# Performance work log

Measured on AMD Instinct MI355X. Metric: run time of the kernel, lower is better.

Reference implementation:

```python
import jax, jax.numpy as jnp
import numpy as np

RATIOS = (0.5, 1.0, 2.0)
SCALES = (8.0, 16.0, 32.0)
BASE = 7.0
FEAT = 16
N_PRE = 6000    # pre-NMS top-k (test-mode default of standard ProposalCreator)
N_POST = 300    # post-NMS proposals per image (fixed -> jit-safe padded output)
NMS_T = 0.7
MIN_SIZE = 16.0
SCALE = 1.0     # forward arg `scale` default
NA = 9          # len(ratios)*len(anchor_scales)


def anchor_base():
    ab = np.zeros((NA, 4), np.float32)
    for i, r in enumerate(RATIOS):
        for j, s in enumerate(SCALES):
            h = BASE * s * np.sqrt(r)
            w = BASE * s * np.sqrt(1.0 / r)
            k = i * len(SCALES) + j
            ab[k] = [BASE / 2 - h / 2, BASE / 2 - w / 2, BASE / 2 + h / 2, BASE / 2 + w / 2]
    return jnp.asarray(ab)


def enum_anchors(H, W):
    # positions-major ordering: (H*W, 9, 4) -> (H*W*9, 4), matching permute(0,2,3,1)
    ab = anchor_base()
    sy = jnp.arange(H, dtype=jnp.float32) * FEAT
    sx = jnp.arange(W, dtype=jnp.float32) * FEAT
    ys, xs = jnp.meshgrid(sy, sx, indexing='ij')
    shift = jnp.stack([ys.ravel(), xs.ravel(), ys.ravel(), xs.ravel()], axis=1)
    return (shift[:, None, :] + ab[None, :, :]).reshape(-1, 4)


def conv2d(x, w, b, pad):
    y = jax.lax.conv_general_dilated(x, w, (1, 1), pad,
                                     dimension_numbers=('NCHW', 'OIHW', 'NCHW'))
    return y + b[None, :, None, None]


def decode(anchors, loc):
    ah = anchors[:, 2] - anchors[:, 0]
    aw = anchors[:, 3] - anchors[:, 1]
    acy = anchors[:, 0] + 0.5 * ah
    acx = anchors[:, 1] + 0.5 * aw
    dy, dx, dh, dw = loc[:, 0], loc[:, 1], loc[:, 2], loc[:, 3]
    cy = dy * ah + acy
    cx = dx * aw + acx
    h = jnp.exp(dh) * ah
    w = jnp.exp(dw) * aw
    return jnp.stack([cy - 0.5 * h, cx - 0.5 * w, cy + 0.5 * h, cx + 0.5 * w], axis=1)


def iou_matrix(b):
    tl = jnp.maximum(b[:, None, :2], b[None, :, :2])
    br = jnp.minimum(b[:, None, 2:], b[None, :, 2:])
    inter = jnp.prod(jnp.clip(br - tl, 0.0, None), axis=-1)
    area = jnp.prod(b[:, 2:] - b[:, :2], axis=-1)
    return inter / (area[:, None] + area[None, :] - inter + 1e-9)


def propose(loc, fg, anchors, img_h, img_w):
    boxes = decode(anchors, loc)
    boxes = jnp.stack([jnp.clip(boxes[:, 0], 0.0, img_h),
                       jnp.clip(boxes[:, 1], 0.0, img_w),
                       jnp.clip(boxes[:, 2], 0.0, img_h),
                       jnp.clip(boxes[:, 3], 0.0, img_w)], axis=1)
    hs = boxes[:, 2] - boxes[:, 0]
    ws = boxes[:, 3] - boxes[:, 1]
    ms = MIN_SIZE * SCALE
    valid = (hs >= ms) & (ws >= ms)
    score = jnp.where(valid, fg, -jnp.inf)
    _, idx = jax.lax.top_k(score, N_PRE)          # sorted by score desc
    bk = boxes[idx]                                # [N_PRE, 4]
    iou = iou_matrix(bk)                           # [N_PRE, N_PRE]

    def body(suppr, xs):
        row, i = xs
        keep_i = jnp.logical_not(suppr[i])
        suppr = suppr | (keep_i & (row > NMS_T) & (jnp.arange(N_PRE) > i))
        return suppr, None

    suppr, _ = jax.lax.scan(body, jnp.zeros(N_PRE, bool), (iou, jnp.arange(N_PRE)))
    keep = jnp.logical_not(suppr)
    # kept boxes first (already score-ordered), padded with trailing boxes
    sel = jnp.argsort(jnp.where(keep, jnp.arange(N_PRE), N_PRE))[:N_POST]
    return bk[sel]


def setup_inputs():
    key = jax.random.key(0)
    ks = jax.random.split(key, 4)
    N, C, H, W = 8, 256, 64, 64
    mid = 256
    return {
        'x': jax.random.normal(ks[0], (N, C, H, W), jnp.float32),
        'conv1_w': jax.random.normal(ks[1], (mid, C, 3, 3), jnp.float32) * 0.02,
        'conv1_b': jnp.zeros((mid,), jnp.float32),
        'score_w': jax.random.normal(ks[2], (NA * 2, mid, 1, 1), jnp.float32) * 0.02,
        'score_b': jnp.zeros((NA * 2,), jnp.float32),
        'loc_w': jax.random.normal(ks[3], (NA * 4, mid, 1, 1), jnp.float32) * 0.02,
        'loc_b': jnp.zeros((NA * 4,), jnp.float32),
        'img_h': 1024,
        'img_w': 1024,
    }


def reference(x, conv1_w, conv1_b, score_w, score_b, loc_w, loc_b, img_h, img_w):
    N, _, H, W = x.shape
    h = jax.nn.relu(conv2d(x, conv1_w, conv1_b, 'SAME'))
    rpn_loc = conv2d(h, loc_w, loc_b, 'VALID')
    rpn_score = conv2d(h, score_w, score_b, 'VALID')
    anchors = enum_anchors(H, W)                                 # [H*W*9, 4]
    rpn_loc = rpn_loc.transpose(0, 2, 3, 1).reshape(N, -1, 4)    # [N, A, 4]
    rpn_score = rpn_score.transpose(0, 2, 3, 1)                  # [N, H, W, 18]
    sm = jax.nn.softmax(rpn_score.reshape(N, H, W, NA, 2), axis=-1)
    fg = sm[..., 1].reshape(N, -1)                               # [N, A]
    rpn_score = rpn_score.reshape(N, -1, 2)
    fh, fw = float(img_h), float(img_w)
    rois = jax.lax.map(lambda a: propose(a[0], a[1], anchors, fh, fw),
                       (rpn_loc, fg)).reshape(-1, 4)             # [N*N_POST, 4]
    roi_indices = jnp.repeat(jnp.arange(N), N_POST)
    return rpn_loc, rpn_score, rois, roi_indices, anchors
```

## Files before the change

kernel.cpp:

```cpp
#include <hip/hip_runtime.h>
#include <cstdint>
#include <cstddef>

#define NBATCH 8
#define MID 256
#define HIMG 64
#define WIMG 64
#define NA 9
#define NPRE 6000
#define NPOST 300
#define NANCH (HIMG*WIMG*NA)
#define NWORDS 94
#define GCOLS 6016
#define LOROWS 16

#define OUT_LOC   0
#define OUT_SCORE 1179648
#define OUT_ROIS  1769472
#define OUT_RIDX  1779072
#define OUT_ANCH  1781472

#define H_OFF    0ul
#define H_BYTES  (8ul*256*64*64*4)
#define WT_OFF   (H_OFF + H_BYTES)
#define WT_BYTES (2304ul*256*4)
#define BOX_OFF  (WT_OFF + WT_BYTES)
#define BOX_BYTES (8ul*36864*4*4)
#define U_OFF    (BOX_OFF + BOX_BYTES)
#define U_BYTES  (8ul*36864*4)
#define CK_OFF   (U_OFF + U_BYTES)
#define CK_BYTES (8ul*8192*8)
#define CC_OFF   (CK_OFF + CK_BYTES)
#define CC_BYTES 64ul
#define BK_OFF   (CC_OFF + CC_BYTES)
#define BK_BYTES (8ul*6000*16)
#define M_OFF    (BK_OFF + BK_BYTES + 64)
#define M_BYTES  (8ul*NWORDS*GCOLS*8)

typedef _Float16 f16x8 __attribute__((ext_vector_type(8)));
typedef _Float16 f16x4 __attribute__((ext_vector_type(4)));
typedef float f32x16 __attribute__((ext_vector_type(16)));

__global__ __launch_bounds__(256) void k_prep_w(const float* __restrict__ w,
                                                _Float16* __restrict__ w3h,
                                                _Float16* __restrict__ w3l) {
    int idx = blockIdx.x * 256 + threadIdx.x;
    if (idx >= 589824) return;
    int e  = idx & 7;
    int t  = idx >> 3;
    int oc = t & 255; t >>= 8;
    int g  = t & 1;   t >>= 1;
    int kb = t & 15;  t >>= 4;
    int s  = t;
    int ic = kb * 16 + g * 8 + e;
    float v = w[(oc * 256 + ic) * 9 + s] * 64.0f;
    _Float16 vh = (_Float16)v;
    float r = v - (float)vh;
    w3h[idx] = vh;
    w3l[idx] = (_Float16)r;
}

__global__ void k_anchors(float* __restrict__ out, unsigned int* __restrict__ cc) {
    int idx = blockIdx.x * 256 + threadIdx.x;
    if (blockIdx.x == 0 && threadIdx.x < 16) cc[threadIdx.x] = 0u;
    if (idx >= NANCH) return;
    int p = idx / 9, a = idx - p * 9;
    int y = p >> 6, xg = p & 63;
    double rr = (a < 3) ? 0.5 : ((a < 6) ? 1.0 : 2.0);
    int sj = a % 3;
    double ssc = (sj == 0) ? 8.0 : ((sj == 1) ? 16.0 : 32.0);
    double hh = 7.0 * ssc * sqrt(rr);
    double ww = 7.0 * ssc * sqrt(1.0 / rr);
    float a0 = (float)(3.5 - 0.5 * hh), a2 = (float)(3.5 + 0.5 * hh);
    float b0 = (float)(3.5 - 0.5 * ww), b2 = (float)(3.5 + 0.5 * ww);
    float* dst = out + OUT_ANCH + (size_t)idx * 4;
    dst[0] = y * 16.0f + a0;
    dst[1] = xg * 16.0f + b0;
    dst[2] = y * 16.0f + a2;
    dst[3] = xg * 16.0f + b2;
}

__global__ __launch_bounds__(1024) void k_conv1m(const float* __restrict__ x,
                                                 const _Float16* __restrict__ w3h,
                                                 const _Float16* __restrict__ w3l,
                                                 const float* __restrict__ bias,
                                                 float* __restrict__ h) {
    __shared__ __align__(16) _Float16 bt0[4 * 66 * 26];
    __shared__ __align__(16) _Float16 bt1[4 * 66 * 26];
    __shared__ float bsh[256];

    const int tid = threadIdx.x;
    const int lane = tid & 63;
    const int wv = tid >> 6;
    const int ocg = wv >> 1;
    const int wn = wv & 1;
    const int y0 = blockIdx.x * 2;
    const int n  = blockIdx.y;
    const int bl31 = lane & 31;
    const int g = lane >> 5;

    for (int i = tid; i < 858; i += 1024) {
        ((f16x8*)bt0)[i] = (f16x8){};
        ((f16x8*)bt1)[i] = (f16x8){};
    }
    if (tid < 256) bsh[tid] = bias[tid];

    f32x16 acc[2];
#pragma unroll
    for (int j = 0; j < 2; ++j)
#pragma unroll
        for (int e = 0; e < 16; ++e) acc[j][e] = 0.0f;

    const int scol = lane;
    const int sr   = wv & 3;
    const int sg   = wv >> 2;
    const int sgy  = y0 - 1 + sr;
    const bool gyok = (sgy >= 0) && (sgy < 64);
    const float* xrow = x + (size_t)n * 1048576 + sgy * 64 + scol;
    const int bto = (sr * 66 + scol + 1) * 26 + sg * 4;

    const int aoffl = (g * 256 + ocg * 32 + bl31) * 8;
    const _Float16* wph = w3h + aoffl;
    const _Float16* wpl = w3l + aoffl;

    float xr[4];
#pragma unroll
    for (int q = 0; q < 4; ++q)
        xr[q] = gyok ? xrow[(size_t)(sg * 4 + q) * 4096] : 0.0f;

    f16x8 AhC = *(const f16x8*)(wph);
    f16x8 AlC = *(const f16x8*)(wpl);

    for (int kb = 0; kb < 16; ++kb) {
        __syncthreads();
        {
            f16x4 hh, hl;
#pragma unroll
            for (int q = 0; q < 4; ++q) {
                float v = xr[q] * 64.0f;
                _Float16 vh = (_Float16)v;
                hh[q] = vh;
                hl[q] = (_Float16)(v - (float)vh);
            }
            *(f16x4*)&bt0[bto] = hh;
            *(f16x4*)&bt1[bto] = hl;
        }
        __syncthreads();
        if (kb < 15) {
#pragma unroll
            for (int q = 0; q < 4; ++q)
                xr[q] = gyok ? xrow[(size_t)((kb + 1) * 16 + sg * 4 + q) * 4096] : 0.0f;
        }

        const int ent00 = wn * 66 + bl31;
        f16x8 Bh0C = *(const f16x8*)&bt0[ent00 * 26 + g * 8];
        f16x8 Bl0C = *(const f16x8*)&bt1[ent00 * 26 + g * 8];
        f16x8 Bh1C = *(const f16x8*)&bt0[(ent00 + 32) * 26 + g * 8];
        f16x8 Bl1C = *(const f16x8*)&bt1[(ent00 + 32) * 26 + g * 8];

        const int kbn_base = (kb < 15) ? (kb + 1) : 15;
#pragma unroll
        for (int s = 0; s < 9; ++s) {
            const int sn  = (s == 8) ? 0 : (s + 1);
            const int kbn = (s == 8) ? kbn_base : kb;
            const _Float16* phn = wph + (size_t)kbn * 4096 + (size_t)sn * 65536;
            const _Float16* pln = wpl + (size_t)kbn * 4096 + (size_t)sn * 65536;
            f16x8 AhN = *(const f16x8*)(phn);
            f16x8 AlN = *(const f16x8*)(pln);

            f16x8 Bh0N = Bh0C, Bl0N = Bl0C, Bh1N = Bh1C, Bl1N = Bl1C;
            if (s < 8) {
                const int dyn = sn / 3 - 1, dxn = sn % 3 - 1;
                const int entn = (wn + dyn + 1) * 66 + dxn + 1 + bl31;
                const int en0 = entn * 26 + g * 8;
                const int en1 = (entn + 32) * 26 + g * 8;
                Bh0N = *(const f16x8*)&bt0[en0];
                Bl0N = *(const f16x8*)&bt1[en0];
                Bh1N = *(const f16x8*)&bt0[en1];
                Bl1N = *(const f16x8*)&bt1[en1];
            }

            __builtin_amdgcn_s_setprio(1);
            acc[0] = __builtin_amdgcn_mfma_f32_32x32x16_f16(AhC, Bh0C, acc[0], 0, 0, 0);
            acc[1] = __builtin_amdgcn_mfma_f32_32x32x16_f16(AhC, Bh1C, acc[1], 0, 0, 0);
            acc[0] = __builtin_amdgcn_mfma_f32_32x32x16_f16(AhC, Bl0C, acc[0], 0, 0, 0);
            acc[1] = __builtin_amdgcn_mfma_f32_32x32x16_f16(AhC, Bl1C, acc[1], 0, 0, 0);
            acc[0] = __builtin_amdgcn_mfma_f32_32x32x16_f16(AlC, Bh0C, acc[0], 0, 0, 0);
            acc[1] = __builtin_amdgcn_mfma_f32_32x32x16_f16(AlC, Bh1C, acc[1], 0, 0, 0);
            __builtin_amdgcn_s_setprio(0);

            AhC = AhN; AlC = AlN;
            Bh0C = Bh0N; Bl0C = Bl0N; Bh1C = Bh1N; Bl1C = Bl1N;
        }
    }

    const int colw = lane & 31;
    const int rgh = (lane >> 5) * 4;
    float* hn = h + (size_t)n * 1048576 + (size_t)(y0 + wn) * 64;
#pragma unroll
    for (int pcb = 0; pcb < 2; ++pcb)
#pragma unroll
        for (int reg = 0; reg < 16; ++reg) {
            const int row = (reg & 3) + 8 * (reg >> 2) + rgh;
            const int oc = ocg * 32 + row;
            float v = acc[pcb][reg] * 2.44140625e-4f + bsh[oc];
            hn[(size_t)oc * 4096 + pcb * 32 + colw] = fmaxf(v, 0.0f);
        }
}

__global__ __launch_bounds__(256) void k_heads(const float* __restrict__ h,
                                               const float* __restrict__ loc_w,
                                               const float* __restrict__ score_w,
                                               const float* __restrict__ loc_b,
                                               const float* __restrict__ score_b,
                                               const int* __restrict__ ihp,
                                               const int* __restrict__ iwp,
                                               float* __restrict__ out,
                                               float* __restrict__ boxes,
                                               unsigned int* __restrict__ ubuf) {
    __shared__ float Wl[54 * 64];
    __shared__ float outb[128 * 57];
    const int tid = threadIdx.x;
    const int pl = tid & 127, chalf = tid >> 7;
    const int c0 = chalf * 27;
    const int ptile = blockIdx.x;
    const int n = blockIdx.y;
    const int pg = ptile * 128 + pl;

    float acc[27];
#pragma unroll
    for (int i = 0; i < 27; ++i) acc[i] = 0.f;

    for (int kc = 0; kc < 4; ++kc) {
        __syncthreads();
        for (int idx = tid; idx < 54 * 64; idx += 256) {
            int c = idx >> 6, kk = idx & 63;
            int gk = kc * 64 + kk;
            Wl[idx] = (c < 36) ? loc_w[c * 256 + gk] : score_w[(c - 36) * 256 + gk];
        }
        __syncthreads();
        for (int k4 = 0; k4 < 64; k4 += 4) {
            int gk = kc * 64 + k4;
            float hv0 = h[(n * 256 + gk + 0) * 4096 + pg];
            float hv1 = h[(n * 256 + gk + 1) * 4096 + pg];
            float hv2 = h[(n * 256 + gk + 2) * 4096 + pg];
            float hv3 = h[(n * 256 + gk + 3) * 4096 + pg];
#pragma unroll
            for (int ci = 0; ci < 27; ++ci) {
                float4 w4 = *(const float4*)&Wl[(c0 + ci) * 64 + k4];
                acc[ci] += hv0 * w4.x + hv1 * w4.y + hv2 * w4.z + hv3 * w4.w;
            }
        }
    }
#pragma unroll
    for (int ci = 0; ci < 27; ++ci) {
        int c = c0 + ci;
        float bv = (c < 36) ? loc_b[c] : score_b[c - 36];
        outb[pl * 57 + c] = acc[ci] + bv;
    }
    __syncthreads();

    const float fh = (float)(*ihp), fwid = (float)(*iwp);
    for (int slot = tid; slot < 128 * 9; slot += 256) {
        int pli = slot / 9, a = slot - pli * 9;
        int p = ptile * 128 + pli;
        int y = p >> 6, xg = p & 63;
        float l0 = outb[pli * 57 + a * 4 + 0];
        float l1 = outb[pli * 57 + a * 4 + 1];
        float l2 = outb[pli * 57 + a * 4 + 2];
        float l3 = outb[pli * 57 + a * 4 + 3];
        float s0 = outb[pli * 57 + 36 + a * 2 + 0];
        float s1 = outb[pli * 57 + 36 + a * 2 + 1];
        size_t base = (size_t)n * NANCH + (size_t)p * 9 + a;
        ((float4*)(out + OUT_LOC))[base] = make_float4(l0, l1, l2, l3);
        ((float2*)(out + OUT_SCORE))[base] = make_float2(s0, s1);
        float mx = fmaxf(s0, s1);
        float e0 = expf(s0 - mx), e1 = expf(s1 - mx);
        float fg = e1 / (e0 + e1);
        double rr = (a < 3) ? 0.5 : ((a < 6) ? 1.0 : 2.0);
        int sj = a % 3;
        double ssc = (sj == 0) ? 8.0 : ((sj == 1) ? 16.0 : 32.0);
        double hhd = 7.0 * ssc * sqrt(rr);
        double wwd = 7.0 * ssc * sqrt(1.0 / rr);
        float a0 = (float)(3.5 - 0.5 * hhd), a2 = (float)(3.5 + 0.5 * hhd);
        float b0 = (float)(3.5 - 0.5 * wwd), b2 = (float)(3.5 + 0.5 * wwd);
        float ay1 = y * 16.0f + a0, ay2 = y * 16.0f + a2;
        float ax1 = xg * 16.0f + b0, ax2 = xg * 16.0f + b2;
        float ah = ay2 - ay1, aw = ax2 - ax1;
        float acy = ay1 + 0.5f * ah, acx = ax1 + 0.5f * aw;
        float cy = l0 * ah + acy, cx = l1 * aw + acx;
        float bh = expf(l2) * ah, bw = expf(l3) * aw;
        float y1 = fminf(fmaxf(cy - 0.5f * bh, 0.f), fh);
        float x1 = fminf(fmaxf(cx - 0.5f * bw, 0.f), fwid);
        float y2 = fminf(fmaxf(cy + 0.5f * bh, 0.f), fh);
        float x2 = fminf(fmaxf(cx + 0.5f * bw, 0.f), fwid);
        ((float4*)boxes)[base] = make_float4(y1, x1, y2, x2);
        bool valid = ((y2 - y1) >= 16.0f) && ((x2 - x1) >= 16.0f);
        float sc = valid ? fg : -__builtin_inff();
        unsigned int ub = __float_as_uint(sc);
        ub = (ub & 0x80000000u) ? ~ub : (ub | 0x80000000u);
        ubuf[base] = ub;
    }
}

__global__ __launch_bounds__(1024) void k_select(const unsigned int* __restrict__ ubuf,
                                                 unsigned long long* __restrict__ ckeys,
                                                 unsigned int* __restrict__ cc) {
    __shared__ unsigned int hist[256];
    __shared__ unsigned int selb;
    __shared__ int rank_s;
    __shared__ unsigned int lcnt;
    const int tid = threadIdx.x;
    const int lane = tid & 63;
    const int b = blockIdx.x;
    const unsigned int* ub = ubuf + (size_t)b * NANCH;
    if (tid == 0) { rank_s = NPRE - 1; lcnt = 0; }
    unsigned int prefix = 0;
    for (int pass = 0; pass < 4; ++pass) {
        int shift = 24 - 8 * pass;
        if (tid < 256) hist[tid] = 0;
        __syncthreads();
        for (int i = tid; i < NANCH; i += 1024) {
            unsigned int u = ub[i];
            bool ok = (pass == 0) || ((u >> (shift + 8)) == (prefix >> (shift + 8)));
            unsigned int byt = (u >> shift) & 255u;
            if (pass == 0) {
                unsigned long long todo = __ballot(ok);
                while (todo) {
                    int src = __builtin_ctzll(todo);
                    unsigned int bb = __shfl(byt, src, 64);
                    unsigned long long m = __ballot(ok && (byt == bb));
                    if (lane == src) atomicAdd(&hist[bb], (unsigned int)__popcll(m));
                    todo &= ~m;
                }
            } else {
                if (ok) atomicAdd(&hist[byt], 1u);
            }
        }
        __syncthreads();
        const int r = rank_s;
        for (int off = 1; off < 256; off <<= 1) {
            unsigned int v = 0;
            if (tid < 256 && tid + off < 256) v = hist[tid + off];
            __syncthreads();
            if (tid < 256) hist[tid] += v;
            __syncthreads();
        }
        if (tid < 256) {
            unsigned int inc = hist[tid];
            unsigned int above = (tid == 255) ? 0u : hist[tid + 1];
            if ((int)inc > r && (int)above <= r) {
                selb = (unsigned int)tid;
                rank_s = r - (int)above;
            }
        }
        __syncthreads();
        prefix |= (selb << shift);
        __syncthreads();
    }
    const unsigned int ustar = prefix;
    for (int i = tid; i < NANCH; i += 1024) {
        unsigned int u = ub[i];
        bool sel2 = (u >= ustar);
        unsigned long long m = __ballot(sel2);
        if (m) {
            int src = __builtin_ctzll(m);
            unsigned int base2 = 0;
            if (lane == src) base2 = atomicAdd(&lcnt, (unsigned int)__popcll(m));
            base2 = __shfl(base2, src, 64);
            if (sel2) {
                unsigned int pos = base2 + (unsigned int)__popcll(m & ((1ull << lane) - 1ull));
                if (pos < 8192)
                    ckeys[(size_t)b * 8192 + pos] =
                        ((unsigned long long)u << 32) | (unsigned int)(0xFFFFFFFFu - (unsigned int)i);
            }
        }
    }
    __syncthreads();
    if (tid == 0) cc[b] = (lcnt > 8192u) ? 8192u : lcnt;
}

__device__ __forceinline__ void cswap_u64(unsigned long long& a, unsigned long long& c, bool desc) {
    bool sw = desc ? (a < c) : (a > c);
    unsigned long long t0 = sw ? c : a;
    unsigned long long t1 = sw ? a : c;
    a = t0; c = t1;
}
__device__ __forceinline__ void net8(unsigned long long v[8], bool d) {
    cswap_u64(v[0], v[4], d); cswap_u64(v[1], v[5], d); cswap_u64(v[2], v[6], d); cswap_u64(v[3], v[7], d);
    cswap_u64(v[0], v[2], d); cswap_u64(v[1], v[3], d); cswap_u64(v[4], v[6], d); cswap_u64(v[5], v[7], d);
    cswap_u64(v[0], v[1], d); cswap_u64(v[2], v[3], d); cswap_u64(v[4], v[5], d); cswap_u64(v[6], v[7], d);
}
__device__ __forceinline__ unsigned long long shfl_xor_u64(unsigned long long x, int lmask) {
    unsigned int lo = (unsigned int)x, hi = (unsigned int)(x >> 32);
    lo = __shfl_xor(lo, lmask, 64);
    hi = __shfl_xor(hi, lmask, 64);
    return ((unsigned long long)hi << 32) | lo;
}

__global__ __launch_bounds__(256) void k_sort_loc(unsigned long long* __restrict__ ckeys,
                                                  const unsigned int* __restrict__ cc) {
    __shared__ unsigned long long S[2048];
    const int tid = threadIdx.x;
    const int seg = blockIdx.x;
    const int b = blockIdx.y;
    const int cnt = (int)cc[b];
    const int gbase = seg * 2048 + tid * 8;
    const int lb = tid * 8;
    unsigned long long* ck = ckeys + (size_t)b * 8192;

    unsigned long long v[8];
#pragma unroll
    for (int e = 0; e < 8; ++e) {
        int i = gbase + e;
        v[e] = (i < cnt) ? ck[i] : 0ull;
    }
    cswap_u64(v[0], v[1], true);  cswap_u64(v[2], v[3], false);
    cswap_u64(v[4], v[5], true);  cswap_u64(v[6], v[7], false);
    cswap_u64(v[0], v[2], true);  cswap_u64(v[1], v[3], true);
    cswap_u64(v[4], v[6], false); cswap_u64(v[5], v[7], false);
    cswap_u64(v[0], v[1], true);  cswap_u64(v[2], v[3], true);
    cswap_u64(v[4], v[5], false); cswap_u64(v[6], v[7], false);
    net8(v, (gbase & 8) == 0);

    for (int k = 16; k <= 2048; k <<= 1) {
        for (int j = k >> 1; j >= 8; j >>= 1) {
            const bool keep_max = (((gbase & k) == 0) != ((gbase & j) != 0));
            if (j >= 512) {
                __syncthreads();
#pragma unroll
                for (int e = 0; e < 8; ++e) S[lb + e] = v[e];
                __syncthreads();
                const int pb = lb ^ j;
#pragma unroll
                for (int e = 0; e < 8; ++e) {
                    unsigned long long p = S[pb + e];
                    v[e] = keep_max ? (v[e] >= p ? v[e] : p) : (v[e] <= p ? v[e] : p);
                }
            } else {
                const int lmask = j >> 3;
#pragma unroll
                for (int e = 0; e < 8; ++e) {
                    unsigned long long p = shfl_xor_u64(v[e], lmask);
                    v[e] = keep_max ? (v[e] >= p ? v[e] : p) : (v[e] <= p ? v[e] : p);
                }
            }
        }
        net8(v, (gbase & k) == 0);
    }
#pragma unroll
    for (int e = 0; e < 8; ++e) ck[gbase + e] = v[e];
}

__global__ __launch_bounds__(256) void k_sort_gmerge(unsigned long long* __restrict__ ckeys,
                                                     int j, int k) {
    const int t = blockIdx.x * 256 + threadIdx.x;
    const int b = blockIdx.y;
    const int i = ((t & ~(j - 1)) << 1) | (t & (j - 1));
    const int l = i | j;
    unsigned long long* ck = ckeys + (size_t)b * 8192;
    unsigned long long a = ck[i], c = ck[l];
    const bool desc = ((i & k) == 0);
    bool sw = desc ? (a < c) : (a > c);
    if (sw) { ck[i] = c; ck[l] = a; }
}

__global__ __launch_bounds__(256) void k_sort_tail(unsigned long long* __restrict__ ckeys,
                                                   int k,
                                                   const float* __restrict__ boxes,
                                                   float* __restrict__ bk,
                                                   int dogather) {
    __shared__ unsigned long long S[2048];
    const int tid = threadIdx.x;
    const int seg = blockIdx.x;
    const int b = blockIdx.y;
    const int gbase = seg * 2048 + tid * 8;
    const int lb = tid * 8;
    unsigned long long* ck = ckeys + (size_t)b * 8192;

    unsigned long long v[8];
#pragma unroll
    for (int e = 0; e < 8; ++e) v[e] = ck[gbase + e];

    for (int j = 1024; j >= 8; j >>= 1) {
        const bool keep_max = (((gbase & k) == 0) != ((gbase & j) != 0));
        if (j >= 512) {
            __syncthreads();
#pragma unroll
            for (int e = 0; e < 8; ++e) S[lb + e] = v[e];
            __syncthreads();
            const int pb = lb ^ j;
#pragma unroll
            for (int e = 0; e < 8; ++e) {
                unsigned long long p = S[pb + e];
                v[e] = keep_max ? (v[e] >= p ? v[e] : p) : (v[e] <= p ? v[e] : p);
            }
        } else {
            const int lmask = j >> 3;
#pragma unroll
            for (int e = 0; e < 8; ++e) {
                unsigned long long p = shfl_xor_u64(v[e], lmask);
                v[e] = keep_max ? (v[e] >= p ? v[e] : p) : (v[e] <= p ? v[e] : p);
            }
        }
    }
    net8(v, (gbase & k) == 0);

    if (!dogather) {
#pragma unroll
        for (int e = 0; e < 8; ++e) ck[gbase + e] = v[e];
    } else {
#pragma unroll
        for (int e = 0; e < 8; ++e) {
            int i = gbase + e;
            if (i < NPRE) {
                unsigned int idx = 0xFFFFFFFFu - (unsigned int)(v[e] & 0xFFFFFFFFull);
                if (idx >= NANCH) idx = NANCH - 1;
                float4 bx = ((const float4*)boxes)[(size_t)b * NANCH + idx];
                ((float4*)bk)[(size_t)b * NPRE + i] = bx;
            }
        }
    }
}

__global__ __launch_bounds__(256) void k_mask(const float* __restrict__ bk,
                                              unsigned long long* __restrict__ MT,
                                              const unsigned int* __restrict__ cc,
                                              int iwbase, int checkdone) {
    const int iw = iwbase + blockIdx.x;
    const int gb = blockIdx.y;
    const int b = blockIdx.z;
    if (checkdone && cc[8 + b] != 0u) return;
    if (iw > 4 * gb + 3) return;
    const int tid = threadIdx.x;
    __shared__ float4 jb[64];
    __shared__ float ja[64];
    if (tid < 64) {
        int j = iw * 64 + tid;
        float4 v = (j < NPRE) ? ((const float4*)bk)[(size_t)b * NPRE + j]
                              : make_float4(0.f, 0.f, 0.f, 0.f);
        jb[tid] = v;
        ja[tid] = (v.z - v.x) * (v.w - v.y);
    }
    __syncthreads();
    const int g = gb * 256 + tid;
    float4 bi = (g < NPRE) ? ((const float4*)bk)[(size_t)b * NPRE + g]
                           : make_float4(0.f, 0.f, 0.f, 0.f);
    float ai = (bi.z - bi.x) * (bi.w - bi.y);
    const double MD = (double)0.7f + 0x1p-25;
    unsigned long long word = 0ull;
#pragma unroll 8
    for (int jj = 0; jj < 64; ++jj) {
        float4 bj = jb[jj];
        float aj = ja[jj];
        float ty = fmaxf(bi.x, bj.x), tx = fmaxf(bi.y, bj.y);
        float by = fminf(bi.z, bj.z), bx = fminf(bi.w, bj.w);
        float ihh = fmaxf(by - ty, 0.f), iww = fmaxf(bx - tx, 0.f);
        float inter = ihh * iww;
        float den = ai + aj - inter + 1e-9f;
        if ((double)inter >= MD * (double)den) word |= (1ull << jj);
    }
    if (g < GCOLS)
        MT[((size_t)b * NWORDS + iw) * GCOLS + g] = word;
}

__global__ __launch_bounds__(1024) void k_nms_try(const unsigned long long* __restrict__ MT,
                                                  const float* __restrict__ bk,
                                                  float* __restrict__ out,
                                                  unsigned int* __restrict__ cc) {
    const int b = blockIdx.x;
    const int tid = threadIdx.x;
    const int lane = tid & 63;
    __shared__ unsigned long long keptw[NWORDS];
    __shared__ unsigned long long dead[LOROWS];
    __shared__ int sel[NPOST];
    __shared__ int totkept;
    const unsigned long long* mtb = MT + (size_t)b * NWORDS * GCOLS;

    for (int i = tid; i < NWORDS; i += 1024) keptw[i] = 0ull;
    if (tid < LOROWS) dead[tid] = 0ull;
    if (tid == 0) totkept = 0;
    __syncthreads();

    for (int c = 0; c < LOROWS; ++c) {
        if (tid < 64) {
            const int g = c * 64 + lane;
            unsigned long long diag = mtb[(size_t)c * GCOLS + g];
            bool deadl = (((dead[c] >> lane) & 1ull) != 0ull) || (g >= NPRE);
            unsigned long long undec = ~__ballot(deadl);
            unsigned long long kc = 0ull;
            while (undec) {
                int i = __builtin_ctzll(undec);
                kc |= (1ull << i);
                unsigned long long supm = __ballot((diag >> i) & 1ull);
                undec &= ~(supm | (1ull << i));
            }
            if (lane == 0) { keptw[c] = kc; totkept += __popcll(kc); }
        }
        __syncthreads();
        if (totkept >= NPOST) break;
        const unsigned long long kc = keptw[c];
        if (kc) {
            for (int g2 = (c + 1) * 64 + tid; g2 < LOROWS * 64; g2 += 1024) {
                unsigned long long w = mtb[(size_t)c * GCOLS + g2] & kc;
                unsigned long long m = __ballot(w != 0ull);
                if (lane == 0 && m) atomicOr(&dead[g2 >> 6], m);
            }
        }
        __syncthreads();
    }

    const int done = (totkept >= NPOST) ? 1 : 0;
    if (tid == 0) cc[8 + b] = (unsigned int)done;
    if (!done) return;

    if (tid == 0) {
        int pos = 0;
        for (int w = 0; w < NWORDS && pos < NPOST; ++w) {
            unsigned long long kw = keptw[w];
            while (kw && pos < NPOST) {
                int i2 = __builtin_ctzll(kw);
                sel[pos++] = w * 64 + i2;
                kw &= kw - 1;
            }
        }
    }
    __syncthreads();
    for (int s2 = tid; s2 < NPOST; s2 += 1024) {
        int i = sel[s2];
        float4 bx = ((const float4*)bk)[(size_t)b * NPRE + i];
        ((float4*)(out + OUT_ROIS))[b * NPOST + s2] = bx;
        out[OUT_RIDX + b * NPOST + s2] = (float)b;
    }
}

__global__ __launch_bounds__(1024) void k_nms_full(const unsigned long long* __restrict__ MT,
                                                   const float* __restrict__ bk,
                                                   float* __restrict__ out,
                                                   const unsigned int* __restrict__ cc) {
    const int b = blockIdx.x;
    if (cc[8 + b] != 0u) return;
    const int tid = threadIdx.x;
    const int lane = tid & 63;
    __shared__ unsigned long long keptw[NWORDS];
    __shared__ unsigned long long dead[NWORDS];
    __shared__ int sel[NPOST];
    __shared__ int totkept;
    const unsigned long long* mtb = MT + (size_t)b * NWORDS * GCOLS;

    for (int i = tid; i < NWORDS; i += 1024) { dead[i] = 0ull; keptw[i] = 0ull; }
    if (tid == 0) totkept = 0;
    __syncthreads();

    for (int c = 0; c < NWORDS; ++c) {
        if (tid < 64) {
            const int g = c * 64 + lane;
            unsigned long long diag = mtb[(size_t)c * GCOLS + g];
            bool deadl = (((dead[c] >> lane) & 1ull) != 0ull) || (g >= NPRE);
            unsigned long long undec = ~__ballot(deadl);
            unsigned long long kc = 0ull;
            while (undec) {
                int i = __builtin_ctzll(undec);
                kc |= (1ull << i);
                unsigned long long supm = __ballot((diag >> i) & 1ull);
                undec &= ~(supm | (1ull << i));
            }
            if (lane == 0) { keptw[c] = kc; totkept += __popcll(kc); }
        }
        __syncthreads();
        if (totkept >= NPOST) break;
        const unsigned long long kc = keptw[c];
        if (kc) {
            for (int g2 = (c + 1) * 64 + tid; g2 < GCOLS; g2 += 1024) {
                unsigned long long w = mtb[(size_t)c * GCOLS + g2] & kc;
                unsigned long long m = __ballot(w != 0ull);
                if (lane == 0 && m) atomicOr(&dead[g2 >> 6], m);
            }
        }
        __syncthreads();
    }

    if (tid == 0) {
        int pos = 0;
        for (int w = 0; w < NWORDS && pos < NPOST; ++w) {
            unsigned long long kw = keptw[w];
            while (kw && pos < NPOST) {
                int i2 = __builtin_ctzll(kw);
                sel[pos++] = w * 64 + i2;
                kw &= kw - 1;
            }
        }
        for (int w = 0; w < NWORDS && pos < NPOST; ++w) {
            int nvalid = NPRE - w * 64; if (nvalid > 64) nvalid = 64;
            unsigned long long vm = (nvalid >= 64) ? ~0ull : ((1ull << nvalid) - 1ull);
            unsigned long long sw = (~keptw[w]) & vm;
            while (sw && pos < NPOST) {
                int i2 = __builtin_ctzll(sw);
                sel[pos++] = w * 64 + i2;
                sw &= sw - 1;
            }
        }
    }
    __syncthreads();
    for (int s2 = tid; s2 < NPOST; s2 += 1024) {
        int i = sel[s2];
        float4 bx = ((const float4*)bk)[(size_t)b * NPRE + i];
        ((float4*)(out + OUT_ROIS))[b * NPOST + s2] = bx;
        out[OUT_RIDX + b * NPOST + s2] = (float)b;
    }
}

extern "C" void kernel_launch(void* const* d_in, const int* in_sizes, int n_in,
                              void* d_out, int out_size, void* d_ws, size_t ws_size,
                              hipStream_t stream) {
    const float* x = (const float*)d_in[0];
    const float* conv1_w = (const float*)d_in[1];
    const float* conv1_b = (const float*)d_in[2];
    const float* score_w = (const float*)d_in[3];
    const float* score_b = (const float*)d_in[4];
    const float* loc_w = (const float*)d_in[5];
    const float* loc_b = (const float*)d_in[6];
    const int* ihp = (const int*)d_in[7];
    const int* iwp = (const int*)d_in[8];
    float* out = (float*)d_out;
    char* ws = (char*)d_ws;
    float* h = (float*)(ws + H_OFF);
    _Float16* w3h = (_Float16*)(ws + WT_OFF);
    _Float16* w3l = (_Float16*)(ws + WT_OFF + 1179648ul);
    float* boxes = (float*)(ws + BOX_OFF);
    unsigned int* ubuf = (unsigned int*)(ws + U_OFF);
    unsigned long long* ckeys = (unsigned long long*)(ws + CK_OFF);
    unsigned int* cc = (unsigned int*)(ws + CC_OFF);
    float* bk = (float*)(ws + BK_OFF);
    unsigned long long* MT = (unsigned long long*)(ws + M_OFF);

    hipLaunchKernelGGL(k_prep_w, dim3(2304), dim3(256), 0, stream, conv1_w, w3h, w3l);
    hipLaunchKernelGGL(k_anchors, dim3(144), dim3(256), 0, stream, out, cc);
    hipLaunchKernelGGL(k_conv1m, dim3(32, 8), dim3(1024), 0, stream, x, w3h, w3l, conv1_b, h);
    hipLaunchKernelGGL(k_heads, dim3(32, 8), dim3(256), 0, stream,
                       h, loc_w, score_w, loc_b, score_b, ihp, iwp, out, boxes, ubuf);
    hipLaunchKernelGGL(k_select, dim3(8), dim3(1024), 0, stream, ubuf, ckeys, cc);
    hipLaunchKernelGGL(k_sort_loc, dim3(4, 8), dim3(256), 0, stream, ckeys, cc);
    hipLaunchKernelGGL(k_sort_gmerge, dim3(16, 8), dim3(256), 0, stream, ckeys, 2048, 4096);
    hipLaunchKernelGGL(k_sort_tail, dim3(4, 8), dim3(256), 0, stream, ckeys, 4096, boxes, bk, 0);
    hipLaunchKernelGGL(k_sort_gmerge, dim3(16, 8), dim3(256), 0, stream, ckeys, 4096, 8192);
    hipLaunchKernelGGL(k_sort_gmerge, dim3(16, 8), dim3(256), 0, stream, ckeys, 2048, 8192);
    hipLaunchKernelGGL(k_sort_tail, dim3(4, 8), dim3(256), 0, stream, ckeys, 8192, boxes, bk, 1);
    hipLaunchKernelGGL(k_mask, dim3(LOROWS, 24, 8), dim3(256), 0, stream, bk, MT, cc, 0, 0);
    hipLaunchKernelGGL(k_nms_try, dim3(8), dim3(1024), 0, stream, MT, bk, out, cc);
    hipLaunchKernelGGL(k_mask, dim3(NWORDS - LOROWS, 24, 8), dim3(256), 0, stream, bk, MT, cc, LOROWS, 1);
    hipLaunchKernelGGL(k_nms_full, dim3(8), dim3(1024), 0, stream, MT, bk, out, cc);
}
```

Measured before the change: 440.4 us.

## Move 1x1 RPN head convolutions onto split-fp16 MFMA matrix cores

Replaces the scalar FP32 FMA loop of the loc/score head kernel with 32x32x16 fp16 MFMA instructions. Each operand is split into high and low fp16 halves, and three products are summed to approximate FP32 accuracy. Head weights are pre-split in the weight-prep kernel into a workspace region reused from the sort-key buffer, padded to 64 output channels. The aim is to cut the ALU-bound head GEMM time, at the cost of some padding waste, extra LDS staging of activations, and a small accuracy deviation from the split-precision scheme.

```diff
diff --git a/kernel.cpp b/kernel.cpp
--- a/kernel.cpp
+++ b/kernel.cpp
@@ -42,22 +42,39 @@
 typedef float f32x16 __attribute__((ext_vector_type(16)));
 
 __global__ __launch_bounds__(256) void k_prep_w(const float* __restrict__ w,
+                                                const float* __restrict__ loc_w,
+                                                const float* __restrict__ score_w,
                                                 _Float16* __restrict__ w3h,
-                                                _Float16* __restrict__ w3l) {
+                                                _Float16* __restrict__ w3l,
+                                                _Float16* __restrict__ whh,
+                                                _Float16* __restrict__ whl) {
     int idx = blockIdx.x * 256 + threadIdx.x;
-    if (idx >= 589824) return;
-    int e  = idx & 7;
-    int t  = idx >> 3;
-    int oc = t & 255; t >>= 8;
-    int g  = t & 1;   t >>= 1;
-    int kb = t & 15;  t >>= 4;
-    int s  = t;
-    int ic = kb * 16 + g * 8 + e;
-    float v = w[(oc * 256 + ic) * 9 + s] * 64.0f;
-    _Float16 vh = (_Float16)v;
-    float r = v - (float)vh;
-    w3h[idx] = vh;
-    w3l[idx] = (_Float16)r;
+    if (idx < 589824) {
+        int e  = idx & 7;
+        int t  = idx >> 3;
+        int oc = t & 255; t >>= 8;
+        int g  = t & 1;   t >>= 1;
+        int kb = t & 15;  t >>= 4;
+        int s  = t;
+        int ic = kb * 16 + g * 8 + e;
+        float v = w[(oc * 256 + ic) * 9 + s] * 64.0f;
+        _Float16 vh = (_Float16)v;
+        w3h[idx] = vh;
+        w3l[idx] = (_Float16)(v - (float)vh);
+    } else if (idx < 589824 + 16384) {
+        int j = idx - 589824;
+        int e  = j & 7;
+        int c  = (j >> 3) & 63;
+        int g  = (j >> 9) & 1;
+        int kb = j >> 10;
+        int k  = kb * 16 + g * 8 + e;
+        float v = (c < 36) ? loc_w[c * 256 + k]
+                 : ((c < 54) ? score_w[(c - 36) * 256 + k] : 0.0f);
+        v *= 64.0f;
+        _Float16 vh = (_Float16)v;
+        whh[j] = vh;
+        whl[j] = (_Float16)(v - (float)vh);
+    }
 }
 
 __global__ void k_anchors(float* __restrict__ out, unsigned int* __restrict__ cc) {
@@ -208,56 +225,85 @@
         }
 }
 
-__global__ __launch_bounds__(256) void k_heads(const float* __restrict__ h,
-                                               const float* __restrict__ loc_w,
-                                               const float* __restrict__ score_w,
-                                               const float* __restrict__ loc_b,
-                                               const float* __restrict__ score_b,
-                                               const int* __restrict__ ihp,
-                                               const int* __restrict__ iwp,
-                                               float* __restrict__ out,
-                                               float* __restrict__ boxes,
-                                               unsigned int* __restrict__ ubuf) {
-    __shared__ float Wl[54 * 64];
+__global__ __launch_bounds__(256) void k_headsm(const float* __restrict__ h,
+                                                const _Float16* __restrict__ whh,
+                                                const _Float16* __restrict__ whl,
+                                                const float* __restrict__ loc_b,
+                                                const float* __restrict__ score_b,
+                                                const int* __restrict__ ihp,
+                                                const int* __restrict__ iwp,
+                                                float* __restrict__ out,
+                                                float* __restrict__ boxes,
+                                                unsigned int* __restrict__ ubuf) {
+    __shared__ __align__(16) _Float16 bt0[128 * 18];
+    __shared__ __align__(16) _Float16 bt1[128 * 18];
     __shared__ float outb[128 * 57];
+    __shared__ float bsh[54];
     const int tid = threadIdx.x;
-    const int pl = tid & 127, chalf = tid >> 7;
-    const int c0 = chalf * 27;
+    const int lane = tid & 63;
+    const int wv = tid >> 6;
+    const int wm = wv >> 1;
+    const int wpx = wv & 1;
     const int ptile = blockIdx.x;
     const int n = blockIdx.y;
-    const int pg = ptile * 128 + pl;
-
-    float acc[27];
-#pragma unroll
-    for (int i = 0; i < 27; ++i) acc[i] = 0.f;
-
-    for (int kc = 0; kc < 4; ++kc) {
-        __syncthreads();
-        for (int idx = tid; idx < 54 * 64; idx += 256) {
-            int c = idx >> 6, kk = idx & 63;
-            int gk = kc * 64 + kk;
-            Wl[idx] = (c < 36) ? loc_w[c * 256 + gk] : score_w[(c - 36) * 256 + gk];
-        }
-        __syncthreads();
-        for (int k4 = 0; k4 < 64; k4 += 4) {
-            int gk = kc * 64 + k4;
-            float hv0 = h[(n * 256 + gk + 0) * 4096 + pg];
-            float hv1 = h[(n * 256 + gk + 1) * 4096 + pg];
-            float hv2 = h[(n * 256 + gk + 2) * 4096 + pg];
-            float hv3 = h[(n * 256 + gk + 3) * 4096 + pg];
-#pragma unroll
-            for (int ci = 0; ci < 27; ++ci) {
-                float4 w4 = *(const float4*)&Wl[(c0 + ci) * 64 + k4];
-                acc[ci] += hv0 * w4.x + hv1 * w4.y + hv2 * w4.z + hv3 * w4.w;
-            }
-        }
-    }
-#pragma unroll
-    for (int ci = 0; ci < 27; ++ci) {
-        int c = c0 + ci;
-        float bv = (c < 36) ? loc_b[c] : score_b[c - 36];
-        outb[pl * 57 + c] = acc[ci] + bv;
-    }
+    const int pxbase = ptile * 128;
+    const int bl31 = lane & 31;
+    const int g = lane >> 5;
+
+    if (tid < 54) bsh[tid] = (tid < 36) ? loc_b[tid] : score_b[tid - 36];
+
+    f32x16 acc[2];
+#pragma unroll
+    for (int j = 0; j < 2; ++j)
+#pragma unroll
+        for (int e = 0; e < 16; ++e) acc[j][e] = 0.0f;
+
+    const int spx = tid >> 1;
+    const int skg = (tid & 1) * 8;
+    const float* hp = h + (size_t)n * 1048576 + pxbase + spx;
+    const int aoff = (g * 64 + wm * 32 + bl31) * 8;
+
+    for (int kb = 0; kb < 16; ++kb) {
+        __syncthreads();
+        {
+            f16x8 hh, hl;
+#pragma unroll
+            for (int q = 0; q < 8; ++q) {
+                float v = hp[(size_t)(kb * 16 + skg + q) * 4096] * 64.0f;
+                _Float16 vh = (_Float16)v;
+                hh[q] = vh;
+                hl[q] = (_Float16)(v - (float)vh);
+            }
+            *(f16x8*)&bt0[spx * 18 + skg] = hh;
+            *(f16x8*)&bt1[spx * 18 + skg] = hl;
+        }
+        __syncthreads();
+        const _Float16* ph = whh + kb * 1024 + aoff;
+        const _Float16* pl = whl + kb * 1024 + aoff;
+        f16x8 Ah = *(const f16x8*)ph;
+        f16x8 Al = *(const f16x8*)pl;
+#pragma unroll
+        for (int j = 0; j < 2; ++j) {
+            const int px = wpx * 64 + j * 32 + bl31;
+            f16x8 Bh = *(const f16x8*)&bt0[px * 18 + g * 8];
+            f16x8 Bl = *(const f16x8*)&bt1[px * 18 + g * 8];
+            acc[j] = __builtin_amdgcn_mfma_f32_32x32x16_f16(Ah, Bh, acc[j], 0, 0, 0);
+            acc[j] = __builtin_amdgcn_mfma_f32_32x32x16_f16(Ah, Bl, acc[j], 0, 0, 0);
+            acc[j] = __builtin_amdgcn_mfma_f32_32x32x16_f16(Al, Bh, acc[j], 0, 0, 0);
+        }
+    }
+
+#pragma unroll
+    for (int j = 0; j < 2; ++j)
+#pragma unroll
+        for (int reg = 0; reg < 16; ++reg) {
+            const int row = (reg & 3) + 8 * (reg >> 2) + (g << 2);
+            const int c = wm * 32 + row;
+            if (c < 54) {
+                const int px = wpx * 64 + j * 32 + bl31;
+                outb[px * 57 + c] = acc[j][reg] * 2.44140625e-4f + bsh[c];
+            }
+        }
     __syncthreads();
 
     const float fh = (float)(*ihp), fwid = (float)(*iwp);
@@ -733,12 +779,15 @@
     unsigned int* cc = (unsigned int*)(ws + CC_OFF);
     float* bk = (float*)(ws + BK_OFF);
     unsigned long long* MT = (unsigned long long*)(ws + M_OFF);
-
-    hipLaunchKernelGGL(k_prep_w, dim3(2304), dim3(256), 0, stream, conv1_w, w3h, w3l);
+    _Float16* whh = (_Float16*)(ws + CK_OFF);
+    _Float16* whl = (_Float16*)(ws + CK_OFF + 32768ul);
+
+    hipLaunchKernelGGL(k_prep_w, dim3(2368), dim3(256), 0, stream,
+                       conv1_w, loc_w, score_w, w3h, w3l, whh, whl);
     hipLaunchKernelGGL(k_anchors, dim3(144), dim3(256), 0, stream, out, cc);
     hipLaunchKernelGGL(k_conv1m, dim3(32, 8), dim3(1024), 0, stream, x, w3h, w3l, conv1_b, h);
-    hipLaunchKernelGGL(k_heads, dim3(32, 8), dim3(256), 0, stream,
-                       h, loc_w, score_w, loc_b, score_b, ihp, iwp, out, boxes, ubuf);
+    hipLaunchKernelGGL(k_headsm, dim3(32, 8), dim3(256), 0, stream,
+                       h, whh, whl, loc_b, score_b, ihp, iwp, out, boxes, ubuf);
     hipLaunchKernelGGL(k_select, dim3(8), dim3(1024), 0, stream, ubuf, ckeys, cc);
     hipLaunchKernelGGL(k_sort_loc, dim3(4, 8), dim3(256), 0, stream, ckeys, cc);
     hipLaunchKernelGGL(k_sort_gmerge, dim3(16, 8), dim3(256), 0, stream, ckeys, 2048, 4096);
```

New measurement: 401.3 us, median of 2. -8.9%, faster.
